# Optimization experiments

Measured on AMD Instinct MI355X. Metric: run time of the kernel, lower is better.

## Reference

```python
import jax, jax.numpy as jnp
import numpy as np

# Model config (matches init_kwargs)
EMBED_DIM = 512
POS_DIM = 192
NUM_HEADS = 8
Q_HEAD = 32   # query/key head dim
P_HEAD = 4    # positional head dim
IN_PROJ_DIM = (Q_HEAD + Q_HEAD + P_HEAD) * NUM_HEADS  # 544
SEQ_LEN = 512
BATCH = 16


def setup_inputs() -> dict:
    key = jax.random.key(0)
    k1, k2, k3, k4, k5 = jax.random.split(key, 5)
    x = jax.random.normal(k1, (SEQ_LEN, BATCH, EMBED_DIM), dtype=jnp.float32)
    pos_emb = jax.random.normal(k2, (1, 2 * SEQ_LEN - 1, POS_DIM), dtype=jnp.float32)
    key_padding_mask = jnp.zeros((BATCH, SEQ_LEN), dtype=bool)
    # in_proj (ScaledLinear): weight (out,in), bias (out,); initial_scale q_head**-0.25
    W_in = jax.random.normal(k3, (IN_PROJ_DIM, EMBED_DIM), dtype=jnp.float32) * (EMBED_DIM ** -0.5) * (Q_HEAD ** -0.25)
    b_in = jax.random.normal(k4, (IN_PROJ_DIM,), dtype=jnp.float32) * 0.01
    # linear_pos: weight (H*P_HEAD, POS_DIM), no bias, initial_scale 0.05
    W_pos = jax.random.normal(k5, (NUM_HEADS * P_HEAD, POS_DIM), dtype=jnp.float32) * (POS_DIM ** -0.5) * 0.05
    return {"x": x, "pos_emb": pos_emb, "key_padding_mask": key_padding_mask,
            "W_in": W_in, "b_in": b_in, "W_pos": W_pos}


def reference(x, pos_emb, key_padding_mask, W_in, b_in, W_pos):
    S, B, _ = x.shape
    H, Dq, Dp = NUM_HEADS, Q_HEAD, P_HEAD
    qdim = H * Dq

    proj = jnp.einsum('sbe,oe->sbo', x, W_in) + b_in            # (S,B,544)
    q = proj[..., :qdim].reshape(S, B, H, Dq)
    k = proj[..., qdim:2 * qdim].reshape(S, B, H, Dq)           # whiten/balance are eval no-ops
    p = proj[..., 2 * qdim:].reshape(S, B, H, Dp)

    # content scores: (H,B,S_tgt,S_src)
    attn_scores = jnp.einsum('sbhd,tbhd->hbst', q, k)

    # positional scores against 2S-1 relative positions
    pe = jnp.einsum('olp,np->oln', pos_emb, W_pos)              # (1, 2S-1, H*Dp)
    pe = pe.reshape(2 * S - 1, H, Dp).transpose(1, 2, 0)        # (H, Dp, 2S-1)
    pos_scores = jnp.einsum('sbhd,hdt->hbst', p, pe)            # (H,B,S,2S-1)

    # relative shift (as_strided trick): out[h,b,i,j] = pos_scores[h,b,i, j - i + S - 1]
    idx = (S - 1) + jnp.arange(S)[None, :] - jnp.arange(S)[:, None]   # (S,S)
    idx = jnp.broadcast_to(idx[None, None], (H, B, S, S))
    pos_scores = jnp.take_along_axis(pos_scores, idx, axis=-1)  # (H,B,S,S)

    attn_scores = attn_scores + pos_scores
    attn_scores = jnp.where(key_padding_mask[None, :, None, :], -1000.0, attn_scores)
    return jax.nn.softmax(attn_scores, axis=-1)
```

## Files before the change

kernel.cpp:

```cpp
#include <hip/hip_runtime.h>

#define SEQ   512
#define BATCH 16
#define EMB   512
#define NH    8
#define DQ    32
#define DP    4
#define OP    544
#define NREL  1023

typedef _Float16 f16;
typedef _Float16 f16x4 __attribute__((ext_vector_type(4)));
typedef _Float16 f16x8 __attribute__((ext_vector_type(8)));
typedef float    f32x4 __attribute__((ext_vector_type(4)));

__global__ __launch_bounds__(256) void k_inproj_mfma(const float* __restrict__ x,
                                                     const float* __restrict__ W,
                                                     const float* __restrict__ bias,
                                                     float* __restrict__ proj) {
    __shared__ f16 Ah[128][72];
    __shared__ f16 Bh[64][72];
    const int tid = threadIdx.x;
    const int m0 = blockIdx.x * 128;
    const int n0 = blockIdx.y * 64;
    const int w  = tid >> 6;
    const int l  = tid & 63;
    const int wm = (w >> 1) * 64;
    const int wn = (w & 1) * 32;
    const int lr = l & 15;
    const int lk = l >> 4;
    const int srow = tid >> 4;
    const int sc4  = (tid & 15) * 4;

    f32x4 acc[4][2];
    #pragma unroll
    for (int mi = 0; mi < 4; mi++)
        #pragma unroll
        for (int ni = 0; ni < 2; ni++) acc[mi][ni] = (f32x4){0.f, 0.f, 0.f, 0.f};

    float4 aReg[8];
    float4 bReg[4];
    #pragma unroll
    for (int it = 0; it < 8; it++)
        aReg[it] = *(const float4*)(x + (size_t)(m0 + it * 16 + srow) * EMB + sc4);
    #pragma unroll
    for (int it = 0; it < 4; it++) {
        int o = n0 + it * 16 + srow;
        bReg[it] = make_float4(0.f, 0.f, 0.f, 0.f);
        if (o < OP) bReg[it] = *(const float4*)(W + (size_t)o * EMB + sc4);
    }

    for (int k0 = 0; k0 < EMB; k0 += 64) {
        #pragma unroll
        for (int it = 0; it < 8; it++) {
            f16x4 hv = {(f16)aReg[it].x, (f16)aReg[it].y, (f16)aReg[it].z, (f16)aReg[it].w};
            *(f16x4*)&Ah[it * 16 + srow][sc4] = hv;
        }
        #pragma unroll
        for (int it = 0; it < 4; it++) {
            f16x4 hv = {(f16)bReg[it].x, (f16)bReg[it].y, (f16)bReg[it].z, (f16)bReg[it].w};
            *(f16x4*)&Bh[it * 16 + srow][sc4] = hv;
        }
        __syncthreads();
        if (k0 + 64 < EMB) {
            #pragma unroll
            for (int it = 0; it < 8; it++)
                aReg[it] = *(const float4*)(x + (size_t)(m0 + it * 16 + srow) * EMB + (k0 + 64) + sc4);
            #pragma unroll
            for (int it = 0; it < 4; it++) {
                int o = n0 + it * 16 + srow;
                bReg[it] = make_float4(0.f, 0.f, 0.f, 0.f);
                if (o < OP) bReg[it] = *(const float4*)(W + (size_t)o * EMB + (k0 + 64) + sc4);
            }
        }
        #pragma unroll
        for (int ks = 0; ks < 2; ks++) {
            f16x8 bfr[2];
            #pragma unroll
            for (int ni = 0; ni < 2; ni++)
                bfr[ni] = *(const f16x8*)&Bh[wn + ni * 16 + lr][ks * 32 + lk * 8];
            #pragma unroll
            for (int mi = 0; mi < 4; mi++) {
                f16x8 afr = *(const f16x8*)&Ah[wm + mi * 16 + lr][ks * 32 + lk * 8];
                #pragma unroll
                for (int ni = 0; ni < 2; ni++)
                    acc[mi][ni] = __builtin_amdgcn_mfma_f32_16x16x32_f16(afr, bfr[ni], acc[mi][ni], 0, 0, 0);
            }
        }
        __syncthreads();
    }
    #pragma unroll
    for (int ni = 0; ni < 2; ni++) {
        int o = n0 + wn + ni * 16 + lr;
        if (o >= OP) continue;
        float bb = bias[o];
        #pragma unroll
        for (int mi = 0; mi < 4; mi++) {
            int mrow = m0 + wm + mi * 16 + lk * 4;
            #pragma unroll
            for (int j = 0; j < 4; j++)
                proj[(size_t)(mrow + j) * OP + o] = acc[mi][ni][j] + bb;
        }
    }
}

__global__ __launch_bounds__(256) void k_pe(const float* __restrict__ pos_emb,
                                            const float* __restrict__ W_pos,
                                            float* __restrict__ pe) {
    int n  = blockIdx.x * 8 + (threadIdx.x >> 5);
    int hd = threadIdx.x & 31;
    if (n >= NREL) return;
    const float* pr = pos_emb + (size_t)n * 192;
    const float* wr = W_pos + (size_t)hd * 192;
    float s = 0.f;
    #pragma unroll
    for (int p = 0; p < 192; p += 4) {
        float4 a = *(const float4*)(pr + p);
        float4 b = *(const float4*)(wr + p);
        s = fmaf(a.x, b.x, fmaf(a.y, b.y, fmaf(a.z, b.z, fmaf(a.w, b.w, s))));
    }
    int h = hd >> 2, d = hd & 3;
    pe[((size_t)h * NREL + n) * 4 + d] = s;
}

__global__ __launch_bounds__(256, 2) void k_attn_mfma(const float* __restrict__ proj,
                                                      const float* __restrict__ pe,
                                                      const unsigned char* __restrict__ mask,
                                                      float* __restrict__ out) {
    __shared__ f16    Kh[512][40];
    __shared__ f16    Qh[64][40];
    __shared__ float4 pe_win[576];
    __shared__ float4 p_lds[64];
    __shared__ float  m_lds[512];

    const int tid = threadIdx.x;
    const int w  = tid >> 6;
    const int l  = tid & 63;
    const int lr = l & 15;
    const int lk = l >> 4;
    const int bid  = blockIdx.x;
    const int rblk = bid & 7;
    const int hb   = bid >> 3;
    const int b = hb & 15;
    const int h = hb >> 4;
    const int i0 = rblk << 6;

    #pragma unroll
    for (int it = 0; it < 16; it++) {
        int idx = tid + 256 * it;
        int row = idx >> 3;
        int c4  = (idx & 7) << 2;
        float4 v = *(const float4*)(proj + ((size_t)row * BATCH + b) * OP + 256 + h * DQ + c4);
        f16x4 hv = {(f16)v.x, (f16)v.y, (f16)v.z, (f16)v.w};
        *(f16x4*)&Kh[row][c4] = hv;
    }
    #pragma unroll
    for (int it = 0; it < 2; it++) {
        int idx = tid + 256 * it;
        int row = idx >> 3;
        int c4  = (idx & 7) << 2;
        float4 v = *(const float4*)(proj + ((size_t)(i0 + row) * BATCH + b) * OP + h * DQ + c4);
        f16x4 hv = {(f16)v.x, (f16)v.y, (f16)v.z, (f16)v.w};
        *(f16x4*)&Qh[row][c4] = hv;
    }
    if (tid < 64)
        p_lds[tid] = *(const float4*)(proj + ((size_t)(i0 + tid) * BATCH + b) * OP + 512 + h * DP);
    if (tid >= 64 && tid < 192) {
        int t4 = tid - 64;
        uchar4 mv = ((const uchar4*)(mask + b * SEQ))[t4];
        m_lds[t4 * 4 + 0] = mv.x ? 1.f : 0.f;
        m_lds[t4 * 4 + 1] = mv.y ? 1.f : 0.f;
        m_lds[t4 * 4 + 2] = mv.z ? 1.f : 0.f;
        m_lds[t4 * 4 + 3] = mv.w ? 1.f : 0.f;
    }
    {
        const int n_base = 448 - i0;
        #pragma unroll
        for (int q = 0; q < 3; q++) {
            int nn = tid + 256 * q;
            if (nn < 575)
                pe_win[nn] = *(const float4*)(pe + ((size_t)h * NREL + n_base + nn) * 4);
        }
    }
    __syncthreads();

    const int iloc = w * 16 + lr;
    const f16x8 qf = *(const f16x8*)&Qh[iloc][lk * 8];
    const float4 p4 = p_lds[iloc];
    f32x4 acc[32];
    const f32x4 zero = (f32x4){0.f, 0.f, 0.f, 0.f};
    #pragma unroll
    for (int c = 0; c < 32; c++) {
        f16x8 kf = *(const f16x8*)&Kh[c * 16 + lr][lk * 8];
        acc[c] = __builtin_amdgcn_mfma_f32_16x16x32_f16(kf, qf, zero, 0, 0, 0);
    }

    #pragma unroll
    for (int c = 0; c < 32; c++) {
        const int tb = c * 16 + lk * 4;
        #pragma unroll
        for (int j = 0; j < 4; j++) {
            const int t = tb + j;
            float4 pv = pe_win[t - iloc + 63];
            float s = acc[c][j];
            s = fmaf(p4.x, pv.x, s);
            s = fmaf(p4.y, pv.y, s);
            s = fmaf(p4.z, pv.z, s);
            s = fmaf(p4.w, pv.w, s);
            acc[c][j] = (m_lds[t] != 0.f) ? -1000.f : s;
        }
    }

    float mx = -1e30f;
    #pragma unroll
    for (int c = 0; c < 32; c++)
        #pragma unroll
        for (int j = 0; j < 4; j++) mx = fmaxf(mx, acc[c][j]);
    mx = fmaxf(mx, __shfl_xor(mx, 16));
    mx = fmaxf(mx, __shfl_xor(mx, 32));
    float sum = 0.f;
    #pragma unroll
    for (int c = 0; c < 32; c++)
        #pragma unroll
        for (int j = 0; j < 4; j++) {
            float e = __expf(acc[c][j] - mx);
            acc[c][j] = e;
            sum += e;
        }
    sum += __shfl_xor(sum, 16);
    sum += __shfl_xor(sum, 32);
    const float inv = 1.f / sum;

    float* orow = out + (((size_t)(h * BATCH + b)) * SEQ + i0 + iloc) * SEQ;
    #pragma unroll
    for (int c = 0; c < 32; c++) {
        float4 v = make_float4(acc[c][0] * inv, acc[c][1] * inv,
                               acc[c][2] * inv, acc[c][3] * inv);
        *(float4*)(orow + c * 16 + lk * 4) = v;
    }
}

extern "C" void kernel_launch(void* const* d_in, const int* in_sizes, int n_in,
                              void* d_out, int out_size, void* d_ws, size_t ws_size,
                              hipStream_t stream) {
    const float* x        = (const float*)d_in[0];
    const float* pos_emb  = (const float*)d_in[1];
    const unsigned char* mask = (const unsigned char*)d_in[2];
    const float* W_in     = (const float*)d_in[3];
    const float* b_in     = (const float*)d_in[4];
    const float* W_pos    = (const float*)d_in[5];
    float* out = (float*)d_out;

    float* proj = (float*)d_ws;
    float* pe   = proj + (size_t)8192 * OP;

    k_inproj_mfma<<<dim3(64, 9), 256, 0, stream>>>(x, W_in, b_in, proj);
    k_pe<<<dim3(128), 256, 0, stream>>>(pos_emb, W_pos, pe);
    k_attn_mfma<<<dim3(1024), 256, 0, stream>>>(proj, pe, mask, out);
}
```

Baseline: 202.6 us.

## Pre-convert inputs to fp16, store q/k projections in fp16, remap attention blocks

Adds a conversion kernel that writes x and W_in as fp16. The in-projection GEMM then loads fp16 directly, uses smaller 64x64 tiles for more blocks and occupancy, and writes q/k as fp16 with the positional projection in a separate compact fp32 buffer. The attention kernel reads half-width K/Q and remaps block indices so blocks sharing the same K are spread differently across the device. It adds a full extra pass over x and one more launch in exchange for halved projection traffic.

```diff
diff --git a/kernel.cpp b/kernel.cpp
--- a/kernel.cpp
+++ b/kernel.cpp
@@ -10,67 +10,83 @@
 #define NREL  1023
 
 typedef _Float16 f16;
-typedef _Float16 f16x4 __attribute__((ext_vector_type(4)));
 typedef _Float16 f16x8 __attribute__((ext_vector_type(8)));
 typedef float    f32x4 __attribute__((ext_vector_type(4)));
 
-__global__ __launch_bounds__(256) void k_inproj_mfma(const float* __restrict__ x,
-                                                     const float* __restrict__ W,
-                                                     const float* __restrict__ bias,
-                                                     float* __restrict__ proj) {
-    __shared__ f16 Ah[128][72];
+#define NX   (SEQ * BATCH * EMB)
+#define NW   (OP * EMB)
+#define N8   ((NX + NW) / 8)
+
+__global__ __launch_bounds__(256) void k_cvt(const float* __restrict__ x,
+                                             const float* __restrict__ W,
+                                             f16* __restrict__ x_h,
+                                             f16* __restrict__ W_h) {
+    int gid = blockIdx.x * 256 + threadIdx.x;
+    if (gid >= N8) return;
+    size_t g8 = (size_t)gid * 8;
+    const float* src;
+    f16* dst;
+    if (g8 < NX) { src = x + g8; dst = x_h + g8; }
+    else         { src = W + (g8 - NX); dst = W_h + (g8 - NX); }
+    float4 a = *(const float4*)src;
+    float4 b = *(const float4*)(src + 4);
+    f16x8 h = {(f16)a.x, (f16)a.y, (f16)a.z, (f16)a.w,
+               (f16)b.x, (f16)b.y, (f16)b.z, (f16)b.w};
+    *(f16x8*)dst = h;
+}
+
+__global__ __launch_bounds__(256, 4) void k_inproj2(const f16* __restrict__ x_h,
+                                                    const f16* __restrict__ W_h,
+                                                    const float* __restrict__ bias,
+                                                    f16* __restrict__ qk_h,
+                                                    float* __restrict__ p_f) {
+    __shared__ f16 Ah[64][72];
     __shared__ f16 Bh[64][72];
     const int tid = threadIdx.x;
-    const int m0 = blockIdx.x * 128;
+    const int m0 = blockIdx.x * 64;
     const int n0 = blockIdx.y * 64;
     const int w  = tid >> 6;
     const int l  = tid & 63;
-    const int wm = (w >> 1) * 64;
+    const int wm = (w >> 1) * 32;
     const int wn = (w & 1) * 32;
     const int lr = l & 15;
     const int lk = l >> 4;
-    const int srow = tid >> 4;
-    const int sc4  = (tid & 15) * 4;
-
-    f32x4 acc[4][2];
-    #pragma unroll
-    for (int mi = 0; mi < 4; mi++)
+
+    f32x4 acc[2][2];
+    #pragma unroll
+    for (int mi = 0; mi < 2; mi++)
         #pragma unroll
         for (int ni = 0; ni < 2; ni++) acc[mi][ni] = (f32x4){0.f, 0.f, 0.f, 0.f};
 
-    float4 aReg[8];
-    float4 bReg[4];
-    #pragma unroll
-    for (int it = 0; it < 8; it++)
-        aReg[it] = *(const float4*)(x + (size_t)(m0 + it * 16 + srow) * EMB + sc4);
-    #pragma unroll
-    for (int it = 0; it < 4; it++) {
-        int o = n0 + it * 16 + srow;
-        bReg[it] = make_float4(0.f, 0.f, 0.f, 0.f);
-        if (o < OP) bReg[it] = *(const float4*)(W + (size_t)o * EMB + sc4);
+    f16x8 aReg[2], bReg[2];
+    #pragma unroll
+    for (int it = 0; it < 2; it++) {
+        int idx = tid + 256 * it;
+        int row = idx >> 3, c8 = (idx & 7) * 8;
+        aReg[it] = *(const f16x8*)(x_h + (size_t)(m0 + row) * EMB + c8);
+        int o = n0 + row;
+        bReg[it] = (f16x8){0,0,0,0,0,0,0,0};
+        if (o < OP) bReg[it] = *(const f16x8*)(W_h + (size_t)o * EMB + c8);
     }
 
     for (int k0 = 0; k0 < EMB; k0 += 64) {
         #pragma unroll
-        for (int it = 0; it < 8; it++) {
-            f16x4 hv = {(f16)aReg[it].x, (f16)aReg[it].y, (f16)aReg[it].z, (f16)aReg[it].w};
-            *(f16x4*)&Ah[it * 16 + srow][sc4] = hv;
-        }
-        #pragma unroll
-        for (int it = 0; it < 4; it++) {
-            f16x4 hv = {(f16)bReg[it].x, (f16)bReg[it].y, (f16)bReg[it].z, (f16)bReg[it].w};
-            *(f16x4*)&Bh[it * 16 + srow][sc4] = hv;
+        for (int it = 0; it < 2; it++) {
+            int idx = tid + 256 * it;
+            int row = idx >> 3, c8 = (idx & 7) * 8;
+            *(f16x8*)&Ah[row][c8] = aReg[it];
+            *(f16x8*)&Bh[row][c8] = bReg[it];
         }
         __syncthreads();
         if (k0 + 64 < EMB) {
             #pragma unroll
-            for (int it = 0; it < 8; it++)
-                aReg[it] = *(const float4*)(x + (size_t)(m0 + it * 16 + srow) * EMB + (k0 + 64) + sc4);
-            #pragma unroll
-            for (int it = 0; it < 4; it++) {
-                int o = n0 + it * 16 + srow;
-                bReg[it] = make_float4(0.f, 0.f, 0.f, 0.f);
-                if (o < OP) bReg[it] = *(const float4*)(W + (size_t)o * EMB + (k0 + 64) + sc4);
+            for (int it = 0; it < 2; it++) {
+                int idx = tid + 256 * it;
+                int row = idx >> 3, c8 = (idx & 7) * 8;
+                aReg[it] = *(const f16x8*)(x_h + (size_t)(m0 + row) * EMB + (k0 + 64) + c8);
+                int o = n0 + row;
+                bReg[it] = (f16x8){0,0,0,0,0,0,0,0};
+                if (o < OP) bReg[it] = *(const f16x8*)(W_h + (size_t)o * EMB + (k0 + 64) + c8);
             }
         }
         #pragma unroll
@@ -80,7 +96,7 @@
             for (int ni = 0; ni < 2; ni++)
                 bfr[ni] = *(const f16x8*)&Bh[wn + ni * 16 + lr][ks * 32 + lk * 8];
             #pragma unroll
-            for (int mi = 0; mi < 4; mi++) {
+            for (int mi = 0; mi < 2; mi++) {
                 f16x8 afr = *(const f16x8*)&Ah[wm + mi * 16 + lr][ks * 32 + lk * 8];
                 #pragma unroll
                 for (int ni = 0; ni < 2; ni++)
@@ -95,11 +111,14 @@
         if (o >= OP) continue;
         float bb = bias[o];
         #pragma unroll
-        for (int mi = 0; mi < 4; mi++) {
+        for (int mi = 0; mi < 2; mi++) {
             int mrow = m0 + wm + mi * 16 + lk * 4;
             #pragma unroll
-            for (int j = 0; j < 4; j++)
-                proj[(size_t)(mrow + j) * OP + o] = acc[mi][ni][j] + bb;
+            for (int j = 0; j < 4; j++) {
+                float v = acc[mi][ni][j] + bb;
+                if (o < 512) qk_h[(size_t)(mrow + j) * 512 + o] = (f16)v;
+                else         p_f[(size_t)(mrow + j) * 32 + (o - 512)] = v;
+            }
         }
     }
 }
@@ -123,10 +142,11 @@
     pe[((size_t)h * NREL + n) * 4 + d] = s;
 }
 
-__global__ __launch_bounds__(256, 2) void k_attn_mfma(const float* __restrict__ proj,
-                                                      const float* __restrict__ pe,
-                                                      const unsigned char* __restrict__ mask,
-                                                      float* __restrict__ out) {
+__global__ __launch_bounds__(256, 2) void k_attn2(const f16* __restrict__ qk_h,
+                                                  const float* __restrict__ p_f,
+                                                  const float* __restrict__ pe,
+                                                  const unsigned char* __restrict__ mask,
+                                                  float* __restrict__ out) {
     __shared__ f16    Kh[512][40];
     __shared__ f16    Qh[64][40];
     __shared__ float4 pe_win[576];
@@ -138,33 +158,27 @@
     const int l  = tid & 63;
     const int lr = l & 15;
     const int lk = l >> 4;
-    const int bid  = blockIdx.x;
-    const int rblk = bid & 7;
-    const int hb   = bid >> 3;
+    const int wg   = (blockIdx.x & 7) * 128 + (blockIdx.x >> 3);
+    const int rblk = wg & 7;
+    const int hb   = wg >> 3;
     const int b = hb & 15;
     const int h = hb >> 4;
     const int i0 = rblk << 6;
 
     #pragma unroll
-    for (int it = 0; it < 16; it++) {
+    for (int it = 0; it < 8; it++) {
         int idx = tid + 256 * it;
-        int row = idx >> 3;
-        int c4  = (idx & 7) << 2;
-        float4 v = *(const float4*)(proj + ((size_t)row * BATCH + b) * OP + 256 + h * DQ + c4);
-        f16x4 hv = {(f16)v.x, (f16)v.y, (f16)v.z, (f16)v.w};
-        *(f16x4*)&Kh[row][c4] = hv;
-    }
-    #pragma unroll
-    for (int it = 0; it < 2; it++) {
-        int idx = tid + 256 * it;
-        int row = idx >> 3;
-        int c4  = (idx & 7) << 2;
-        float4 v = *(const float4*)(proj + ((size_t)(i0 + row) * BATCH + b) * OP + h * DQ + c4);
-        f16x4 hv = {(f16)v.x, (f16)v.y, (f16)v.z, (f16)v.w};
-        *(f16x4*)&Qh[row][c4] = hv;
+        int row = idx >> 2, c8 = (idx & 3) * 8;
+        f16x8 v = *(const f16x8*)(qk_h + ((size_t)row * BATCH + b) * 512 + 256 + h * DQ + c8);
+        *(f16x8*)&Kh[row][c8] = v;
+    }
+    {
+        int row = tid >> 2, c8 = (tid & 3) * 8;
+        f16x8 v = *(const f16x8*)(qk_h + ((size_t)(i0 + row) * BATCH + b) * 512 + h * DQ + c8);
+        *(f16x8*)&Qh[row][c8] = v;
     }
     if (tid < 64)
-        p_lds[tid] = *(const float4*)(proj + ((size_t)(i0 + tid) * BATCH + b) * OP + 512 + h * DP);
+        p_lds[tid] = *(const float4*)(p_f + ((size_t)(i0 + tid) * BATCH + b) * 32 + h * DP);
     if (tid >= 64 && tid < 192) {
         int t4 = tid - 64;
         uchar4 mv = ((const uchar4*)(mask + b * SEQ))[t4];
@@ -251,10 +265,14 @@
     const float* W_pos    = (const float*)d_in[5];
     float* out = (float*)d_out;
 
-    float* proj = (float*)d_ws;
-    float* pe   = proj + (size_t)8192 * OP;
-
-    k_inproj_mfma<<<dim3(64, 9), 256, 0, stream>>>(x, W_in, b_in, proj);
+    f16*   x_h  = (f16*)d_ws;
+    f16*   W_h  = x_h + NX;
+    f16*   qk_h = W_h + NW;
+    float* p_f  = (float*)(qk_h + (size_t)8192 * 512);
+    float* pe   = p_f + (size_t)8192 * 32;
+
+    k_cvt<<<dim3((N8 + 255) / 256), 256, 0, stream>>>(x, W_in, x_h, W_h);
+    k_inproj2<<<dim3(128, 9), 256, 0, stream>>>(x_h, W_h, b_in, qk_h, p_f);
     k_pe<<<dim3(128), 256, 0, stream>>>(pos_emb, W_pos, pe);
-    k_attn_mfma<<<dim3(1024), 256, 0, stream>>>(proj, pe, mask, out);
-}
+    k_attn2<<<dim3(1024), 256, 0, stream>>>(qk_h, p_f, pe, mask, out);
+}
```

Result: faster. 194.1 us (-4.2%).
